# Kernel tuning notes

Hardware: AMD Instinct MI355X
Metric: run time of the kernel (lower is better)

The kernel has to match this reference:

```python
import jax, jax.numpy as jnp
import numpy as np

B, S, F, D, U, DS = 128, 64, 32, 128, 128, 128  # batch, seq, features, feat_dim, units, static_dim
DIN = S * F * D + DS  # grn_concat input dim
EPS = 1e-3  # keras LayerNormalization default epsilon


def _ln(x, gamma, beta):
    m = jnp.mean(x, axis=-1, keepdims=True)
    v = jnp.mean(jnp.square(x - m), axis=-1, keepdims=True)
    return (x - m) * jax.lax.rsqrt(v + EPS) * gamma + beta


def setup_inputs() -> dict:
    key = jax.random.key(0)
    ks = iter(jax.random.split(key, 32))
    p = lambda *shape: jax.random.normal(next(ks), shape, dtype=jnp.float32) * 0.02
    inp = {
        "inputs": jax.random.normal(next(ks), (B, S, F * D), dtype=jnp.float32),
        "static_input": jax.random.normal(next(ks), (B, DS), dtype=jnp.float32),
        # grn_concat (input dim DIN != U -> project path active)
        "cWe": p(DIN, U), "cbe": jnp.zeros((U,), jnp.float32),
        "cWl": p(U, U), "cbl": jnp.zeros((U,), jnp.float32),
        "cWgl": p(U, U), "cbgl": jnp.zeros((U,), jnp.float32),
        "cWgs": p(U, U), "cbgs": jnp.zeros((U,), jnp.float32),
        "cgamma": jnp.ones((U,), jnp.float32), "cbeta": jnp.zeros((U,), jnp.float32),
        "cWp": p(DIN, U), "cbp": jnp.zeros((U,), jnp.float32),
        # softmax Dense: units -> num_features
        "Ws": p(U, F), "bs": jnp.zeros((F,), jnp.float32),
        # per-feature GRNs, stacked over feature axis (feat_dim == units -> no project)
        "fWe": p(F, D, U), "fbe": jnp.zeros((F, U), jnp.float32),
        "fWl": p(F, U, U), "fbl": jnp.zeros((F, U), jnp.float32),
        "fWgl": p(F, U, U), "fbgl": jnp.zeros((F, U), jnp.float32),
        "fWgs": p(F, U, U), "fbgs": jnp.zeros((F, U), jnp.float32),
        "fgamma": jnp.ones((F, U), jnp.float32), "fbeta": jnp.zeros((F, U), jnp.float32),
    }
    return inp


def reference(inputs, static_input, cWe, cbe, cWl, cbl, cWgl, cbgl, cWgs, cbgs,
              cgamma, cbeta, cWp, cbp, Ws, bs, fWe, fbe, fWl, fbl, fWgl, fbgl,
              fWgs, fbgs, fgamma, fbeta):
    b = inputs.shape[0]
    # --- selection weights: flatten + concat static, grn_concat, softmax dense ---
    v = jnp.concatenate([inputs.reshape(b, -1), static_input], axis=-1)  # [B, DIN]
    h = jax.nn.elu(v @ cWe + cbe)
    h = h @ cWl + cbl
    res = v @ cWp + cbp  # project (DIN != U)
    g = (h @ cWgl + cbgl) * jax.nn.sigmoid(h @ cWgs + cbgs)  # GLU
    y = _ln(res + g, cgamma, cbeta)  # [B, U]
    w = jax.nn.softmax(y @ Ws + bs, axis=-1)  # [B, F]
    # --- per-feature GRNs, batched over feature axis ---
    x = inputs.reshape(b, S, F, D)  # tf.split along axis 2
    h = jax.nn.elu(jnp.einsum('bsfd,fdu->bsfu', x, fWe) + fbe)
    h = jnp.einsum('bsfu,fuv->bsfv', h, fWl) + fbl
    g = (jnp.einsum('bsfu,fuv->bsfv', h, fWgl) + fbgl) * \
        jax.nn.sigmoid(jnp.einsum('bsfu,fuv->bsfv', h, fWgs) + fbgs)
    xg = _ln(x + g, fgamma, fbeta)  # [B, S, F, U]
    # --- softmax-weighted combine (v repeated over seq, matmul transpose_a) ---
    out = jnp.einsum('bf,bsfu->bsu', w, xg)  # [B, S, U]
    return out
```

## Files before the change

### kernel.cpp

```cpp
#include <hip/hip_runtime.h>


typedef unsigned short u16;
typedef __attribute__((ext_vector_type(4))) u16 u16x4;
typedef __attribute__((ext_vector_type(8))) u16 u16x8;
typedef __attribute__((ext_vector_type(8))) __bf16 bf16x8;
typedef __attribute__((ext_vector_type(4))) float f32x4;

__device__ __forceinline__ u16 f2bf(float f) {
  unsigned int x = __float_as_uint(f);
  return (u16)((x + 0x7fffu + ((x >> 16) & 1u)) >> 16);
}
__device__ __forceinline__ float eluf(float x) { return x > 0.f ? x : __expf(x) - 1.f; }
__device__ __forceinline__ float sigmoidf_(float x) { return 1.f / (1.f + __expf(-x)); }

#define MFMA_BF16(a, b, c) __builtin_amdgcn_mfma_f32_16x16x32_bf16((a), (b), (c), 0, 0, 0)

__global__ __launch_bounds__(128) void k0_prep(
    const float* __restrict__ fWe, const float* __restrict__ fWl,
    const float* __restrict__ fWgl, const float* __restrict__ fWgs,
    u16* __restrict__ wT)
{
  const int b = blockIdx.x, f = b >> 2, mat = b & 3;
  const float* srcs[4] = {fWe, fWl, fWgl, fWgs};
  const float* src = srcs[mat] + (size_t)f * 16384;
  u16* dst = wT + (size_t)b * 16384;
  const int n = threadIdx.x;
  for (int k8 = 0; k8 < 16; ++k8) {
    u16x8 p;
#pragma unroll
    for (int j = 0; j < 8; ++j) p[j] = f2bf(src[(k8 * 8 + j) * 128 + n]);
    *(u16x8*)&dst[n * 128 + k8 * 8] = p;
  }
}

__global__ __launch_bounds__(1024) void k1_bigmm(
    const float* __restrict__ inp, const float* __restrict__ cWe,
    const float* __restrict__ cWp, float* __restrict__ outE, float* __restrict__ outP)
{
  __shared__ __align__(16) u16 xA[2][128][72];
  __shared__ __align__(16) u16 wE[2][128][72];
  __shared__ __align__(16) u16 wP[2][128][72];
  const int t = threadIdx.x;
  const int lane = t & 63, wv = t >> 6, quad = lane >> 4, l16 = lane & 15;
  const int mat = wv >> 3, wvm = wv & 7;
  const int wt = t & 511, wmi = t >> 9;
  const int k4g = wt >> 5, nb4 = wt & 31;
  const float* Wm = wmi ? cWp : cWe;

  f32x4 acc[8];
#pragma unroll
  for (int n = 0; n < 8; ++n)
#pragma unroll
    for (int r = 0; r < 4; ++r) acc[n][r] = 0.f;

  const size_t kbase = (size_t)blockIdx.x * 1024;

  float4 avr[2], wvr[4];
  auto load_regs = [&](int it) {
    const size_t kk = kbase + (size_t)it * 64;
#pragma unroll
    for (int i = 0; i < 2; ++i) {
      const int idx = t + i * 1024;
      const int row = idx >> 4, fo = idx & 15;
      avr[i] = *(const float4*)(inp + (size_t)row * 262144 + kk + fo * 4);
    }
#pragma unroll
    for (int j = 0; j < 4; ++j)
      wvr[j] = *(const float4*)(Wm + (kk + (size_t)(k4g * 4 + j)) * 128 + nb4 * 4);
  };
  auto store_lds = [&](int buf) {
#pragma unroll
    for (int i = 0; i < 2; ++i) {
      const int idx = t + i * 1024;
      const int row = idx >> 4, fo = idx & 15;
      u16x4 p; p[0] = f2bf(avr[i].x); p[1] = f2bf(avr[i].y);
      p[2] = f2bf(avr[i].z); p[3] = f2bf(avr[i].w);
      *(u16x4*)&xA[buf][row][fo * 4] = p;
    }
    u16 (*Wl)[72] = wmi ? wP[buf] : wE[buf];
#pragma unroll
    for (int c = 0; c < 4; ++c) {
      u16x4 col;
      col[0] = f2bf(((const float*)&wvr[0])[c]);
      col[1] = f2bf(((const float*)&wvr[1])[c]);
      col[2] = f2bf(((const float*)&wvr[2])[c]);
      col[3] = f2bf(((const float*)&wvr[3])[c]);
      *(u16x4*)&Wl[nb4 * 4 + c][k4g * 4] = col;
    }
  };

  load_regs(0);
  store_lds(0);
  for (int it = 0; it < 16; ++it) {
    const int buf = it & 1;
    __syncthreads();
    if (it < 15) load_regs(it + 1);
    u16 (*Wb)[72] = mat ? wP[buf] : wE[buf];
#pragma unroll
    for (int ks = 0; ks < 2; ++ks) {
      const int ko = ks * 32 + quad * 8;
      const bf16x8 a = *(const bf16x8*)&xA[buf][16 * wvm + l16][ko];
#pragma unroll
      for (int nt = 0; nt < 8; ++nt) {
        const bf16x8 b = *(const bf16x8*)&Wb[nt * 16 + l16][ko];
        acc[nt] = MFMA_BF16(a, b, acc[nt]);
      }
    }
    if (it < 15) store_lds(buf ^ 1);
  }
  float* outp = mat ? outP : outE;
#pragma unroll
  for (int nt = 0; nt < 8; ++nt) {
    const int col = nt * 16 + l16;
#pragma unroll
    for (int r = 0; r < 4; ++r) {
      const int row = 16 * wvm + quad * 4 + r;
      atomicAdd(&outp[row * 128 + col], acc[nt][r]);
    }
  }
}

__global__ __launch_bounds__(512) void k1b_small(
    const float* __restrict__ stat,
    const float* __restrict__ cWe, const float* __restrict__ cbe,
    const float* __restrict__ cWl, const float* __restrict__ cbl,
    const float* __restrict__ cWgl, const float* __restrict__ cbgl,
    const float* __restrict__ cWgs, const float* __restrict__ cbgs,
    const float* __restrict__ cgam, const float* __restrict__ cbet,
    const float* __restrict__ cWp, const float* __restrict__ cbp,
    const float* __restrict__ Ws, const float* __restrict__ bs,
    const float* __restrict__ preE, const float* __restrict__ preP,
    float* __restrict__ wout)
{
  const int b = blockIdx.x, t = threadIdx.x;
  const int u = t & 127, dc = t >> 7;
  __shared__ float shS[128], shA[128], shB[128], par[8][132], red[4];
  if (t < 128) shS[t] = stat[b * 128 + t];
  __syncthreads();

  const float* we = cWe + (size_t)262144 * 128;
  const float* wp = cWp + (size_t)262144 * 128;
  float hp = 0.f, rp = 0.f;
  for (int d = dc * 32; d < dc * 32 + 32; ++d) {
    const float sv = shS[d];
    hp += sv * we[d * 128 + u];
    rp += sv * wp[d * 128 + u];
  }
  par[dc][u] = hp; par[4 + dc][u] = rp;
  __syncthreads();

  float rs = 0.f;
  if (t < 128) {
    const float he = preE[b * 128 + t] + cbe[t] + par[0][t] + par[1][t] + par[2][t] + par[3][t];
    rs = preP[b * 128 + t] + cbp[t] + par[4][t] + par[5][t] + par[6][t] + par[7][t];
    shA[t] = eluf(he);
  }
  __syncthreads();

  float p = 0.f;
  for (int d = dc * 32; d < dc * 32 + 32; ++d) p += shA[d] * cWl[d * 128 + u];
  par[dc][u] = p;
  __syncthreads();
  if (t < 128) shB[t] = cbl[t] + par[0][t] + par[1][t] + par[2][t] + par[3][t];
  __syncthreads();

  float gp = 0.f, sp = 0.f;
  for (int d = dc * 32; d < dc * 32 + 32; ++d) {
    const float hv = shB[d];
    gp += hv * cWgl[d * 128 + u];
    sp += hv * cWgs[d * 128 + u];
  }
  par[dc][u] = gp; par[4 + dc][u] = sp;
  __syncthreads();

  float z = 0.f;
  if (t < 128) {
    const float gl = cbgl[t] + par[0][t] + par[1][t] + par[2][t] + par[3][t];
    const float gs = cbgs[t] + par[4][t] + par[5][t] + par[6][t] + par[7][t];
    z = rs + gl * sigmoidf_(gs);
  }
  float s = z, q = z * z;
#pragma unroll
  for (int off = 32; off >= 1; off >>= 1) { s += __shfl_xor(s, off); q += __shfl_xor(q, off); }
  if ((t & 63) == 0 && t < 128) { red[(t >> 6) * 2] = s; red[(t >> 6) * 2 + 1] = q; }
  __syncthreads();
  if (t < 128) {
    const float S = red[0] + red[2], Q = red[1] + red[3];
    const float mean = S * (1.f / 128.f);
    const float var = Q * (1.f / 128.f) - mean * mean;
    const float rstd = rsqrtf(var + 1e-3f);
    shA[t] = (z - mean) * rstd * cgam[t] + cbet[t];
  }
  __syncthreads();
  if (t < 32) {
    float sj = bs[t];
    for (int uu = 0; uu < 128; ++uu) sj += shA[uu] * Ws[uu * 32 + t];
    float m = sj;
#pragma unroll
    for (int off = 16; off >= 1; off >>= 1) m = fmaxf(m, __shfl_xor(m, off));
    const float e = __expf(sj - m);
    float se = e;
#pragma unroll
    for (int off = 16; off >= 1; off >>= 1) se += __shfl_xor(se, off);
    wout[b * 32 + t] = e / se;
  }
}

__device__ __forceinline__ void stage_wt(const u16* __restrict__ src, int kh,
                                         u16 WT[][72], int t)
{
#pragma unroll
  for (int i = 0; i < 4; ++i) {
    const int u = t + i * 256;
    const int n = u >> 3, k8 = u & 7;
    *(u16x8*)&WT[n][k8 * 8] = *(const u16x8*)(src + n * 128 + kh + k8 * 8);
  }
}

__device__ __forceinline__ void mm_half(const u16 A[][136], const u16 WT[][72],
                                        int wv, int quad, int l16, int kh, f32x4 acc[8])
{
#pragma unroll
  for (int ks = 0; ks < 2; ++ks) {
    const int kol = ks * 32 + quad * 8;
    const bf16x8 a = *(const bf16x8*)&A[16 * wv + l16][kh + kol];
#pragma unroll
    for (int nt = 0; nt < 8; ++nt) {
      const bf16x8 b = *(const bf16x8*)&WT[nt * 16 + l16][kol];
      acc[nt] = MFMA_BF16(a, b, acc[nt]);
    }
  }
}

__global__ __launch_bounds__(256) void k2_grn(
    const float* __restrict__ inp, const u16* __restrict__ wT,
    const float* __restrict__ fbe, const float* __restrict__ fbl,
    const float* __restrict__ fbgl, const float* __restrict__ fbgs,
    const float* __restrict__ fgam, const float* __restrict__ fbet,
    const float* __restrict__ wsel, float* __restrict__ out)
{
  __shared__ __align__(16) u16 xA[64][136];
  __shared__ __align__(16) u16 hA[64][136];
  __shared__ __align__(16) u16 WT[128][72];
  const int t = threadIdx.x;
  const int lane = t & 63, wv = t >> 6, quad = lane >> 4, l16 = lane & 15;
  const int bb = blockIdx.x & 127, fg = blockIdx.x >> 7;

  f32x4 acc[8], glr[8], racc[8];
#pragma unroll
  for (int n = 0; n < 8; ++n)
#pragma unroll
    for (int r = 0; r < 4; ++r) racc[n][r] = 0.f;

#define ZERO_ACC() do { _Pragma("unroll") \
  for (int n_ = 0; n_ < 8; ++n_) { acc[n_][0]=0.f; acc[n_][1]=0.f; acc[n_][2]=0.f; acc[n_][3]=0.f; } } while (0)

  for (int fi = 0; fi < 8; ++fi) {
    const int f = fg * 8 + fi;
    const float wb = wsel[bb * 32 + f];
    const u16* wf = wT + (size_t)f * 65536;

    __syncthreads();
#pragma unroll
    for (int i = 0; i < 8; ++i) {
      const int u = t + i * 256;
      const int row = u >> 5, fo = u & 31;
      const float4 v = *(const float4*)(inp + (size_t)(bb * 64 + row) * 4096 + f * 128 + fo * 4);
      u16x4 p; p[0] = f2bf(v.x); p[1] = f2bf(v.y); p[2] = f2bf(v.z); p[3] = f2bf(v.w);
      *(u16x4*)&xA[row][fo * 4] = p;
    }

    stage_wt(wf, 0, WT, t);
    __syncthreads();
    ZERO_ACC();
    mm_half(xA, WT, wv, quad, l16, 0, acc);
    __syncthreads();
    stage_wt(wf, 64, WT, t);
    __syncthreads();
    mm_half(xA, WT, wv, quad, l16, 64, acc);
#pragma unroll
    for (int nt = 0; nt < 8; ++nt) {
      const int col = nt * 16 + l16;
      const float bv = fbe[f * 128 + col];
#pragma unroll
      for (int r = 0; r < 4; ++r)
        hA[16 * wv + quad * 4 + r][col] = f2bf(eluf(acc[nt][r] + bv));
    }
    __syncthreads();

    stage_wt(wf + 16384, 0, WT, t);
    __syncthreads();
    ZERO_ACC();
    mm_half(hA, WT, wv, quad, l16, 0, acc);
    __syncthreads();
    stage_wt(wf + 16384, 64, WT, t);
    __syncthreads();
    mm_half(hA, WT, wv, quad, l16, 64, acc);
#pragma unroll
    for (int nt = 0; nt < 8; ++nt) {
      const int col = nt * 16 + l16;
      const float bv = fbl[f * 128 + col];
#pragma unroll
      for (int r = 0; r < 4; ++r)
        hA[16 * wv + quad * 4 + r][col] = f2bf(acc[nt][r] + bv);
    }
    __syncthreads();

    stage_wt(wf + 2 * 16384, 0, WT, t);
    __syncthreads();
    ZERO_ACC();
    mm_half(hA, WT, wv, quad, l16, 0, acc);
    __syncthreads();
    stage_wt(wf + 2 * 16384, 64, WT, t);
    __syncthreads();
    mm_half(hA, WT, wv, quad, l16, 64, acc);
#pragma unroll
    for (int nt = 0; nt < 8; ++nt) {
      const int col = nt * 16 + l16;
      const float bv = fbgl[f * 128 + col];
#pragma unroll
      for (int r = 0; r < 4; ++r) glr[nt][r] = acc[nt][r] + bv;
    }
    __syncthreads();

    stage_wt(wf + 3 * 16384, 0, WT, t);
    __syncthreads();
    ZERO_ACC();
    mm_half(hA, WT, wv, quad, l16, 0, acc);
    __syncthreads();
    stage_wt(wf + 3 * 16384, 64, WT, t);
    __syncthreads();
    mm_half(hA, WT, wv, quad, l16, 64, acc);

#pragma unroll
    for (int nt = 0; nt < 8; ++nt) {
      const int col = nt * 16 + l16;
      const float bv = fbgs[f * 128 + col];
#pragma unroll
      for (int r = 0; r < 4; ++r) {
        const float g = glr[nt][r] * sigmoidf_(acc[nt][r] + bv);
        const float x = __uint_as_float(((unsigned int)xA[16 * wv + quad * 4 + r][col]) << 16);
        acc[nt][r] = x + g;
      }
    }
    float sm[4], sq[4];
#pragma unroll
    for (int r = 0; r < 4; ++r) {
      float s = 0.f, q = 0.f;
#pragma unroll
      for (int nt = 0; nt < 8; ++nt) { const float zz = acc[nt][r]; s += zz; q += zz * zz; }
      sm[r] = s; sq[r] = q;
    }
#pragma unroll
    for (int off = 1; off <= 8; off <<= 1)
#pragma unroll
      for (int r = 0; r < 4; ++r) { sm[r] += __shfl_xor(sm[r], off); sq[r] += __shfl_xor(sq[r], off); }
#pragma unroll
    for (int r = 0; r < 4; ++r) {
      const float mean = sm[r] * (1.f / 128.f);
      const float var = sq[r] * (1.f / 128.f) - mean * mean;
      const float rstd = rsqrtf(var + 1e-3f);
      sm[r] = mean; sq[r] = rstd;
    }
#pragma unroll
    for (int nt = 0; nt < 8; ++nt) {
      const int col = nt * 16 + l16;
      const float gam = fgam[f * 128 + col];
      const float bet = fbet[f * 128 + col];
#pragma unroll
      for (int r = 0; r < 4; ++r) {
        const float xg = (acc[nt][r] - sm[r]) * sq[r] * gam + bet;
        racc[nt][r] += wb * xg;
      }
    }
  }

#pragma unroll
  for (int nt = 0; nt < 8; ++nt) {
    const int col = nt * 16 + l16;
#pragma unroll
    for (int r = 0; r < 4; ++r) {
      const int grow = bb * 64 + 16 * wv + quad * 4 + r;
      atomicAdd(&out[(size_t)grow * 128 + col], racc[nt][r]);
    }
  }
#undef ZERO_ACC
}

extern "C" void kernel_launch(void* const* d_in, const int* in_sizes, int n_in,
                              void* d_out, int out_size, void* d_ws, size_t ws_size,
                              hipStream_t stream)
{
  const float* inp    = (const float*)d_in[0];
  const float* stat   = (const float*)d_in[1];
  const float* cWe    = (const float*)d_in[2];
  const float* cbe    = (const float*)d_in[3];
  const float* cWl    = (const float*)d_in[4];
  const float* cbl    = (const float*)d_in[5];
  const float* cWgl   = (const float*)d_in[6];
  const float* cbgl   = (const float*)d_in[7];
  const float* cWgs   = (const float*)d_in[8];
  const float* cbgs   = (const float*)d_in[9];
  const float* cgamma = (const float*)d_in[10];
  const float* cbeta  = (const float*)d_in[11];
  const float* cWp    = (const float*)d_in[12];
  const float* cbp    = (const float*)d_in[13];
  const float* Ws     = (const float*)d_in[14];
  const float* bs     = (const float*)d_in[15];
  const float* fWe    = (const float*)d_in[16];
  const float* fbe    = (const float*)d_in[17];
  const float* fWl    = (const float*)d_in[18];
  const float* fbl    = (const float*)d_in[19];
  const float* fWgl   = (const float*)d_in[20];
  const float* fbgl   = (const float*)d_in[21];
  const float* fWgs   = (const float*)d_in[22];
  const float* fbgs   = (const float*)d_in[23];
  const float* fgam   = (const float*)d_in[24];
  const float* fbet   = (const float*)d_in[25];

  float* ws_he  = (float*)d_ws;
  float* ws_res = ws_he + 16384;
  float* ws_w   = ws_res + 16384;
  u16*   ws_wT  = (u16*)(ws_w + 4096);

  hipMemsetAsync(d_ws, 0, 32768 * sizeof(float), stream);
  hipMemsetAsync(d_out, 0, (size_t)out_size * sizeof(float), stream);
  k0_prep<<<128, 128, 0, stream>>>(fWe, fWl, fWgl, fWgs, ws_wT);
  k1_bigmm<<<256, 1024, 0, stream>>>(inp, cWe, cWp, ws_he, ws_res);
  k1b_small<<<128, 512, 0, stream>>>(stat, cWe, cbe, cWl, cbl, cWgl, cbgl, cWgs, cbgs,
                                     cgamma, cbeta, cWp, cbp, Ws, bs, ws_he, ws_res, ws_w);
  k2_grn<<<512, 256, 0, stream>>>(inp, ws_wT, fbe, fbl, fbgl, fbgs,
                                  fgam, fbet, ws_w, (float*)d_out);
}
```

Measured before the change: 574.5 us.

## Deepen k1 prefetch, swizzle LDS layout, double-buffer k2 weight staging

In the big GEMM kernel the register prefetch now runs two tiles ahead, and the padded LDS tiles are replaced by XOR-swizzled unpadded tiles with a lighter waitcnt+barrier. This is meant to hide global latency better and avoid bank conflicts. The per-feature GRN kernel double-buffers its weight tiles in LDS and loads the next tile into registers while the MFMAs run, removing about half of its barriers. The prep kernel also uses 512 threads per block instead of 128. In exchange, register pressure rises (two sets of 16 weight floats plus activations), the W loads become scalar and strided, and the swizzle indexing has to be exactly right.

```diff
diff --git a/kernel.cpp b/kernel.cpp
--- a/kernel.cpp
+++ b/kernel.cpp
@@ -16,7 +16,7 @@
 
 #define MFMA_BF16(a, b, c) __builtin_amdgcn_mfma_f32_16x16x32_bf16((a), (b), (c), 0, 0, 0)
 
-__global__ __launch_bounds__(128) void k0_prep(
+__global__ __launch_bounds__(512) void k0_prep(
     const float* __restrict__ fWe, const float* __restrict__ fWl,
     const float* __restrict__ fWgl, const float* __restrict__ fWgs,
     u16* __restrict__ wT)
@@ -25,8 +25,8 @@
   const float* srcs[4] = {fWe, fWl, fWgl, fWgs};
   const float* src = srcs[mat] + (size_t)f * 16384;
   u16* dst = wT + (size_t)b * 16384;
-  const int n = threadIdx.x;
-  for (int k8 = 0; k8 < 16; ++k8) {
+  const int n = threadIdx.x & 127, qc = threadIdx.x >> 7;
+  for (int k8 = qc * 4; k8 < qc * 4 + 4; ++k8) {
     u16x8 p;
 #pragma unroll
     for (int j = 0; j < 8; ++j) p[j] = f2bf(src[(k8 * 8 + j) * 128 + n]);
@@ -38,14 +38,17 @@
     const float* __restrict__ inp, const float* __restrict__ cWe,
     const float* __restrict__ cWp, float* __restrict__ outE, float* __restrict__ outP)
 {
-  __shared__ __align__(16) u16 xA[2][128][72];
-  __shared__ __align__(16) u16 wE[2][128][72];
-  __shared__ __align__(16) u16 wP[2][128][72];
+  __shared__ __align__(16) u16 xA[2][128][64];
+  __shared__ __align__(16) u16 wE[2][128][64];
+  __shared__ __align__(16) u16 wP[2][128][64];
   const int t = threadIdx.x;
   const int lane = t & 63, wv = t >> 6, quad = lane >> 4, l16 = lane & 15;
   const int mat = wv >> 3, wvm = wv & 7;
+  const int arow = t >> 3, af = t & 7;
+  const int aslot = (af ^ (arow & 7)) * 8;
   const int wt = t & 511, wmi = t >> 9;
-  const int k4g = wt >> 5, nb4 = wt & 31;
+  const int wn = wt & 127, wkg = wt >> 7;
+  const int wphi = (wn ^ (wn >> 2)) & 7;
   const float* Wm = wmi ? cWp : cWe;
 
   f32x4 acc[8];
@@ -56,58 +59,66 @@
 
   const size_t kbase = (size_t)blockIdx.x * 1024;
 
-  float4 avr[2], wvr[4];
-  auto load_regs = [&](int it) {
+  float4 av0[2], av1[2];
+  float wv0[16], wv1[16];
+
+  auto load_regs = [&](int it, float4* av, float* wr) {
     const size_t kk = kbase + (size_t)it * 64;
-#pragma unroll
-    for (int i = 0; i < 2; ++i) {
-      const int idx = t + i * 1024;
-      const int row = idx >> 4, fo = idx & 15;
-      avr[i] = *(const float4*)(inp + (size_t)row * 262144 + kk + fo * 4);
-    }
-#pragma unroll
-    for (int j = 0; j < 4; ++j)
-      wvr[j] = *(const float4*)(Wm + (kk + (size_t)(k4g * 4 + j)) * 128 + nb4 * 4);
+    av[0] = *(const float4*)(inp + (size_t)arow * 262144 + kk + af * 8);
+    av[1] = *(const float4*)(inp + (size_t)arow * 262144 + kk + af * 8 + 4);
+#pragma unroll
+    for (int j = 0; j < 16; ++j)
+      wr[j] = Wm[(kk + (size_t)(wkg * 16 + j)) * 128 + wn];
   };
-  auto store_lds = [&](int buf) {
-#pragma unroll
-    for (int i = 0; i < 2; ++i) {
-      const int idx = t + i * 1024;
-      const int row = idx >> 4, fo = idx & 15;
-      u16x4 p; p[0] = f2bf(avr[i].x); p[1] = f2bf(avr[i].y);
-      p[2] = f2bf(avr[i].z); p[3] = f2bf(avr[i].w);
-      *(u16x4*)&xA[buf][row][fo * 4] = p;
-    }
-    u16 (*Wl)[72] = wmi ? wP[buf] : wE[buf];
-#pragma unroll
-    for (int c = 0; c < 4; ++c) {
-      u16x4 col;
-      col[0] = f2bf(((const float*)&wvr[0])[c]);
-      col[1] = f2bf(((const float*)&wvr[1])[c]);
-      col[2] = f2bf(((const float*)&wvr[2])[c]);
-      col[3] = f2bf(((const float*)&wvr[3])[c]);
-      *(u16x4*)&Wl[nb4 * 4 + c][k4g * 4] = col;
+  auto store_lds = [&](int buf, const float4* av, const float* wr) {
+    u16x8 pa;
+    pa[0] = f2bf(av[0].x); pa[1] = f2bf(av[0].y);
+    pa[2] = f2bf(av[0].z); pa[3] = f2bf(av[0].w);
+    pa[4] = f2bf(av[1].x); pa[5] = f2bf(av[1].y);
+    pa[6] = f2bf(av[1].z); pa[7] = f2bf(av[1].w);
+    *(u16x8*)&xA[buf][arow][aslot] = pa;
+    u16 (*Wl)[64] = wmi ? wP[buf] : wE[buf];
+#pragma unroll
+    for (int s = 0; s < 2; ++s) {
+      u16x8 pw;
+#pragma unroll
+      for (int j = 0; j < 8; ++j) pw[j] = f2bf(wr[s * 8 + j]);
+      *(u16x8*)&Wl[wn][((wkg * 2 + s) ^ wphi) * 8] = pw;
     }
   };
 
-  load_regs(0);
-  store_lds(0);
+  load_regs(0, av0, wv0);
+  load_regs(1, av1, wv1);
+  store_lds(0, av0, wv0);
+
+  const int m = 16 * wvm + l16;
+  const int phA = l16 & 7;
+  const int phB = (l16 & 7) ^ (l16 >> 2);
+
   for (int it = 0; it < 16; ++it) {
     const int buf = it & 1;
-    __syncthreads();
-    if (it < 15) load_regs(it + 1);
-    u16 (*Wb)[72] = mat ? wP[buf] : wE[buf];
+    asm volatile("s_waitcnt lgkmcnt(0)" ::: "memory");
+    __builtin_amdgcn_s_barrier();
+    if (it < 14) {
+      if (buf == 0) load_regs(it + 2, av0, wv0);
+      else          load_regs(it + 2, av1, wv1);
+    }
+    const u16 (*Xb)[64] = xA[buf];
+    const u16 (*WbT)[64] = mat ? wP[buf] : wE[buf];
 #pragma unroll
     for (int ks = 0; ks < 2; ++ks) {
-      const int ko = ks * 32 + quad * 8;
-      const bf16x8 a = *(const bf16x8*)&xA[buf][16 * wvm + l16][ko];
+      const int slot = ks * 4 + quad;
+      const bf16x8 a = *(const bf16x8*)&Xb[m][(slot ^ phA) * 8];
 #pragma unroll
       for (int nt = 0; nt < 8; ++nt) {
-        const bf16x8 b = *(const bf16x8*)&Wb[nt * 16 + l16][ko];
+        const bf16x8 b = *(const bf16x8*)&WbT[nt * 16 + l16][(slot ^ phB ^ ((nt & 1) * 4)) * 8];
         acc[nt] = MFMA_BF16(a, b, acc[nt]);
       }
     }
-    if (it < 15) store_lds(buf ^ 1);
+    if (it < 15) {
+      if (buf == 0) store_lds(1, av1, wv1);
+      else          store_lds(0, av0, wv0);
+    }
   }
   float* outp = mat ? outP : outE;
 #pragma unroll
@@ -207,17 +218,6 @@
   }
 }
 
-__device__ __forceinline__ void stage_wt(const u16* __restrict__ src, int kh,
-                                         u16 WT[][72], int t)
-{
-#pragma unroll
-  for (int i = 0; i < 4; ++i) {
-    const int u = t + i * 256;
-    const int n = u >> 3, k8 = u & 7;
-    *(u16x8*)&WT[n][k8 * 8] = *(const u16x8*)(src + n * 128 + kh + k8 * 8);
-  }
-}
-
 __device__ __forceinline__ void mm_half(const u16 A[][136], const u16 WT[][72],
                                         int wv, int quad, int l16, int kh, f32x4 acc[8])
 {
@@ -242,7 +242,7 @@
 {
   __shared__ __align__(16) u16 xA[64][136];
   __shared__ __align__(16) u16 hA[64][136];
-  __shared__ __align__(16) u16 WT[128][72];
+  __shared__ __align__(16) u16 WT[2][128][72];
   const int t = threadIdx.x;
   const int lane = t & 63, wv = t >> 6, quad = lane >> 4, l16 = lane & 15;
   const int bb = blockIdx.x & 127, fg = blockIdx.x >> 7;
@@ -255,6 +255,22 @@
 
 #define ZERO_ACC() do { _Pragma("unroll") \
   for (int n_ = 0; n_ < 8; ++n_) { acc[n_][0]=0.f; acc[n_][1]=0.f; acc[n_][2]=0.f; acc[n_][3]=0.f; } } while (0)
+
+  u16x8 wreg[4];
+  auto wt_load = [&](const u16* src) {
+#pragma unroll
+    for (int i = 0; i < 4; ++i) {
+      const int u = t + i * 256;
+      wreg[i] = *(const u16x8*)(src + (u >> 3) * 128 + (u & 7) * 8);
+    }
+  };
+  auto wt_write = [&](int nb) {
+#pragma unroll
+    for (int i = 0; i < 4; ++i) {
+      const int u = t + i * 256;
+      *(u16x8*)&WT[nb][u >> 3][(u & 7) * 8] = wreg[i];
+    }
+  };
 
   for (int fi = 0; fi < 8; ++fi) {
     const int f = fg * 8 + fi;
@@ -270,15 +286,17 @@
       u16x4 p; p[0] = f2bf(v.x); p[1] = f2bf(v.y); p[2] = f2bf(v.z); p[3] = f2bf(v.w);
       *(u16x4*)&xA[row][fo * 4] = p;
     }
-
-    stage_wt(wf, 0, WT, t);
-    __syncthreads();
+    wt_load(wf);
+    wt_write(0);
+    __syncthreads();
+
+    wt_load(wf + 64);
     ZERO_ACC();
-    mm_half(xA, WT, wv, quad, l16, 0, acc);
-    __syncthreads();
-    stage_wt(wf, 64, WT, t);
-    __syncthreads();
-    mm_half(xA, WT, wv, quad, l16, 64, acc);
+    mm_half(xA, WT[0], wv, quad, l16, 0, acc);
+    wt_write(1);
+    __syncthreads();
+    wt_load(wf + 16384);
+    mm_half(xA, WT[1], wv, quad, l16, 64, acc);
 #pragma unroll
     for (int nt = 0; nt < 8; ++nt) {
       const int col = nt * 16 + l16;
@@ -287,16 +305,16 @@
       for (int r = 0; r < 4; ++r)
         hA[16 * wv + quad * 4 + r][col] = f2bf(eluf(acc[nt][r] + bv));
     }
-    __syncthreads();
-
-    stage_wt(wf + 16384, 0, WT, t);
-    __syncthreads();
+    wt_write(0);
+    __syncthreads();
+
+    wt_load(wf + 16384 + 64);
     ZERO_ACC();
-    mm_half(hA, WT, wv, quad, l16, 0, acc);
-    __syncthreads();
-    stage_wt(wf + 16384, 64, WT, t);
-    __syncthreads();
-    mm_half(hA, WT, wv, quad, l16, 64, acc);
+    mm_half(hA, WT[0], wv, quad, l16, 0, acc);
+    wt_write(1);
+    __syncthreads();
+    wt_load(wf + 2 * 16384);
+    mm_half(hA, WT[1], wv, quad, l16, 64, acc);
 #pragma unroll
     for (int nt = 0; nt < 8; ++nt) {
       const int col = nt * 16 + l16;
@@ -305,33 +323,31 @@
       for (int r = 0; r < 4; ++r)
         hA[16 * wv + quad * 4 + r][col] = f2bf(acc[nt][r] + bv);
     }
-    __syncthreads();
-
-    stage_wt(wf + 2 * 16384, 0, WT, t);
-    __syncthreads();
+    wt_write(0);
+    __syncthreads();
+
+    wt_load(wf + 2 * 16384 + 64);
     ZERO_ACC();
-    mm_half(hA, WT, wv, quad, l16, 0, acc);
-    __syncthreads();
-    stage_wt(wf + 2 * 16384, 64, WT, t);
-    __syncthreads();
-    mm_half(hA, WT, wv, quad, l16, 64, acc);
-#pragma unroll
-    for (int nt = 0; nt < 8; ++nt) {
-      const int col = nt * 16 + l16;
-      const float bv = fbgl[f * 128 + col];
+    mm_half(hA, WT[0], wv, quad, l16, 0, acc);
+    wt_write(1);
+    __syncthreads();
+    wt_load(wf + 3 * 16384);
+    mm_half(hA, WT[1], wv, quad, l16, 64, acc);
+#pragma unroll
+    for (int nt = 0; nt < 8; ++nt) {
+      const float bv = fbgl[f * 128 + nt * 16 + l16];
 #pragma unroll
       for (int r = 0; r < 4; ++r) glr[nt][r] = acc[nt][r] + bv;
     }
-    __syncthreads();
-
-    stage_wt(wf + 3 * 16384, 0, WT, t);
-    __syncthreads();
+    wt_write(0);
+    __syncthreads();
+
+    wt_load(wf + 3 * 16384 + 64);
     ZERO_ACC();
-    mm_half(hA, WT, wv, quad, l16, 0, acc);
-    __syncthreads();
-    stage_wt(wf + 3 * 16384, 64, WT, t);
-    __syncthreads();
-    mm_half(hA, WT, wv, quad, l16, 64, acc);
+    mm_half(hA, WT[0], wv, quad, l16, 0, acc);
+    wt_write(1);
+    __syncthreads();
+    mm_half(hA, WT[1], wv, quad, l16, 64, acc);
 
 #pragma unroll
     for (int nt = 0; nt < 8; ++nt) {
@@ -426,7 +442,7 @@
 
   hipMemsetAsync(d_ws, 0, 32768 * sizeof(float), stream);
   hipMemsetAsync(d_out, 0, (size_t)out_size * sizeof(float), stream);
-  k0_prep<<<128, 128, 0, stream>>>(fWe, fWl, fWgl, fWgs, ws_wT);
+  k0_prep<<<128, 512, 0, stream>>>(fWe, fWl, fWgl, fWgs, ws_wT);
   k1_bigmm<<<256, 1024, 0, stream>>>(inp, cWe, cWp, ws_he, ws_res);
   k1b_small<<<128, 512, 0, stream>>>(stat, cWe, cbe, cWl, cbl, cWgl, cbgl, cWgs, cbgs,
                                      cgamma, cbeta, cWp, cbp, Ws, bs, ws_he, ws_res, ws_w);
```

New measurement: 592.3 us. +3.1%, slower.
